# Kernel optimization log

Measured on AMD Instinct MI355X. Metric: run time of the kernel, lower is better.

Reference implementation:

```python
import jax, jax.numpy as jnp
import numpy as np

BATCH = 131072
NUM_OSC = 4
NUM_SPEC = 300
FREQ_LO, FREQ_HI = 0.5, 5.0


def setup_inputs() -> dict:
    key = jax.random.key(0)
    ks = jax.random.split(key, 8)
    return {
        "G": jax.random.normal(ks[0], (BATCH, 8), dtype=jnp.float32),
        "W1": jax.random.normal(ks[1], (100, 8), dtype=jnp.float32) * 0.3,
        "b1": jax.random.normal(ks[2], (100,), dtype=jnp.float32) * 0.1,
        "W2": jax.random.normal(ks[3], (100, 100), dtype=jnp.float32) * 0.1,
        "b2": jax.random.normal(ks[4], (100,), dtype=jnp.float32) * 0.1,
        "W_w0": jax.random.normal(ks[5], (NUM_OSC, 100), dtype=jnp.float32) * 0.1,
        "W_wp": jax.random.normal(ks[6], (NUM_OSC, 100), dtype=jnp.float32) * 0.1,
        # torch.nn.init.uniform_(lin_g.weight, a=0.0, b=0.1)
        "W_g": jax.random.uniform(ks[7], (NUM_OSC, 100), dtype=jnp.float32) * 0.1,
    }


def reference(G, W1, b1, W2, b2, W_w0, W_wp, W_g):
    # MLP trunk: 8 -> 100 -> 100, ReLU on both layers
    out = jax.nn.relu(G @ W1.T + b1)
    out = jax.nn.relu(out @ W2.T + b2)          # (B, 100)

    # Oscillator parameter heads (bias-free), ReLU-clamped, shape (B, 4, 1)
    w0 = jax.nn.relu(out @ W_w0.T)[:, :, None]
    wp = jax.nn.relu(out @ W_wp.T)[:, :, None]
    g = jax.nn.relu(out @ W_g.T)[:, :, None]

    # Frequency grid (300,) broadcast against (B, 4, 1)
    w = jnp.arange(FREQ_LO, FREQ_HI, (FREQ_HI - FREQ_LO) / NUM_SPEC, dtype=jnp.float32)

    # Lorentz oscillator imaginary permittivity
    num = (wp ** 2) * (w * g)                   # (B, 4, 300)
    den = (w0 ** 2 - w ** 2) ** 2 + (w ** 2) * (g ** 2)
    e2 = num / den
    return jnp.sum(e2, axis=1)                  # (B, 300)
```

## Files before the change

### kernel.cpp

```cpp
#include <hip/hip_runtime.h>

#define BATCH 131072
#define NS    300
#define H     100
#define BLK   256
#define EPB   64
#define NBLK  (BATCH / EPB)
#define NQ4   (EPB * NS / 4)
#define H2STR 112
#define LOOFF 14336

typedef __attribute__((ext_vector_type(8))) short bf16x8;
typedef __attribute__((ext_vector_type(4))) float f32x4;

__device__ __forceinline__ unsigned short f2bf(float f) {
    unsigned int u = __float_as_uint(f);
    return (unsigned short)((u + 0x7fffu + ((u >> 16) & 1u)) >> 16);
}
__device__ __forceinline__ float bf2f(unsigned short h) {
    return __uint_as_float(((unsigned int)h) << 16);
}

__global__ void prep_w2(const float* __restrict__ W2, unsigned short* __restrict__ wsb) {
    const int fi   = blockIdx.x * 4 + (threadIdx.x >> 6);
    const int lane = threadIdx.x & 63;
    const int s = fi / 7, t = fi % 7;
    const int n  = t * 16 + (lane & 15);
    const int k0 = s * 32 + ((lane >> 4) << 3);
    unsigned short* hi = wsb + ((size_t)fi * 64 + lane) * 8;
#pragma unroll
    for (int i = 0; i < 8; ++i) {
        const int k = k0 + i;
        const float v = (k < H && n < H) ? W2[n * H + k] : 0.f;
        const unsigned short h = f2bf(v);
        hi[i]         = h;
        hi[LOOFF + i] = f2bf(v - bf2f(h));
    }
}

__global__ void prep_small(const float* __restrict__ Ww0, const float* __restrict__ Wwp,
                           const float* __restrict__ Wg,  const float* __restrict__ b2,
                           float* __restrict__ hdt, float* __restrict__ b2p) {
    const int i = blockIdx.x * 256 + threadIdx.x;
    if (i < 12 * 112) {
        const int c = i / 112, j = i % 112;
        const float* src = (c < 4) ? Ww0 : (c < 8) ? Wwp : Wg;
        hdt[i] = (j < H) ? src[(c & 3) * H + j] : 0.f;
    }
    if (i < 112) b2p[i] = (i < H) ? b2[i] : 0.f;
}

__global__ __launch_bounds__(BLK)
void lorentz_fused(const float* __restrict__ G,   const float* __restrict__ W1,
                   const float* __restrict__ b1,  const unsigned short* __restrict__ wsb,
                   const float* __restrict__ hdt, const float* __restrict__ b2p,
                   float* __restrict__ out)
{
    __shared__ __align__(16) float h2buf[4][16][H2STR];
    __shared__ __align__(16) float sPP[EPB * 12];

    const int tid  = threadIdx.x;
    const int w    = tid >> 6, lane = tid & 63, ln = lane & 15, gr = lane >> 4;
    const int e0   = blockIdx.x * EPB + w * 16;

    const float4* gp = (const float4*)(G + (size_t)(e0 + ln) * 8);
    const float4 gA = gp[0], gB = gp[1];

    f32x4 acc[7];
#pragma unroll
    for (int t = 0; t < 7; ++t) acc[t] = (f32x4){0.f, 0.f, 0.f, 0.f};

    const bf16x8* Bf = (const bf16x8*)wsb;

#pragma unroll
    for (int s = 0; s < 4; ++s) {
        bf16x8 ahi, alo;
#pragma unroll
        for (int i = 0; i < 8; ++i) {
            const int k  = s * 32 + gr * 8 + i;
            const int kc = (k < H) ? k : (H - 1);
            const float4 ra = ((const float4*)(W1 + kc * 8))[0];
            const float4 rb = ((const float4*)(W1 + kc * 8))[1];
            float s0 = fmaf(gA.x, ra.x, b1[kc]);
            float s1 = gA.y * ra.y;
            s0 = fmaf(gA.z, ra.z, s0);  s1 = fmaf(gA.w, ra.w, s1);
            s0 = fmaf(gB.x, rb.x, s0);  s1 = fmaf(gB.y, rb.y, s1);
            s0 = fmaf(gB.z, rb.z, s0);  s1 = fmaf(gB.w, rb.w, s1);
            const float h = fmaxf(s0 + s1, 0.f);
            const unsigned short hh = f2bf(h);
            ahi[i] = (short)hh;
            alo[i] = (short)f2bf(h - bf2f(hh));
        }
#pragma unroll
        for (int t = 0; t < 7; ++t) {
            const bf16x8 bh = Bf[(s * 7 + t) * 64 + lane];
            const bf16x8 bl = Bf[1792 + (s * 7 + t) * 64 + lane];
            acc[t] = __builtin_amdgcn_mfma_f32_16x16x32_bf16(ahi, bh, acc[t], 0, 0, 0);
            acc[t] = __builtin_amdgcn_mfma_f32_16x16x32_bf16(ahi, bl, acc[t], 0, 0, 0);
            acc[t] = __builtin_amdgcn_mfma_f32_16x16x32_bf16(alo, bh, acc[t], 0, 0, 0);
        }
    }

#pragma unroll
    for (int t = 0; t < 7; ++t) {
        const float b2v = b2p[t * 16 + ln];
#pragma unroll
        for (int r = 0; r < 4; ++r)
            h2buf[w][gr * 4 + r][t * 16 + ln] = fmaxf(acc[t][r] + b2v, 0.f);
    }
    __syncthreads();

    {
        const int row = lane >> 2, q = lane & 3;
        const float4* h4 = (const float4*)&h2buf[w][row][0];
        const float4* d0 = (const float4*)(hdt + q * 112);
        const float4* d1 = (const float4*)(hdt + (4 + q) * 112);
        const float4* d2 = (const float4*)(hdt + (8 + q) * 112);
        float s0 = 0.f, s1 = 0.f, s2 = 0.f;
#pragma unroll
        for (int k4 = 0; k4 < 28; ++k4) {
            const float4 hv = h4[k4];
            const float4 a = d0[k4], b = d1[k4], c = d2[k4];
            s0 = fmaf(hv.x, a.x, s0); s1 = fmaf(hv.x, b.x, s1); s2 = fmaf(hv.x, c.x, s2);
            s0 = fmaf(hv.y, a.y, s0); s1 = fmaf(hv.y, b.y, s1); s2 = fmaf(hv.y, c.y, s2);
            s0 = fmaf(hv.z, a.z, s0); s1 = fmaf(hv.z, b.z, s1); s2 = fmaf(hv.z, c.z, s2);
            s0 = fmaf(hv.w, a.w, s0); s1 = fmaf(hv.w, b.w, s1); s2 = fmaf(hv.w, c.w, s2);
        }
        const float w0 = fmaxf(s0, 0.f), wp = fmaxf(s1, 0.f), gg = fmaxf(s2, 0.f);
        const int el = w * 16 + row;
        sPP[el * 12 + q]     = w0 * w0;
        sPP[el * 12 + 4 + q] = gg * gg;
        sPP[el * 12 + 8 + q] = wp * wp * gg;
    }
    __syncthreads();

    float4* out4 = (float4*)out;
    const size_t base4 = (size_t)blockIdx.x * NQ4;

#define SPEC(idx4)                                                              \
    {   const int e  = (idx4) / 75;                                             \
        const int k4 = (idx4) - e * 75;                                         \
        const float4 P0 = ((const float4*)(sPP + e * 12))[0];                   \
        const float4 P1 = ((const float4*)(sPP + e * 12))[1];                   \
        const float4 P2 = ((const float4*)(sPP + e * 12))[2];                   \
        const float kb = (float)(k4 << 2);                                      \
        float4 r; float* rp = (float*)&r;                                       \
        _Pragma("unroll")                                                       \
        for (int i = 0; i < 4; ++i) {                                           \
            const float w_  = 0.5f + (kb + (float)i) * 0.015f;                  \
            const float wsq = w_ * w_;                                          \
            const float t0 = P0.x - wsq, t1 = P0.y - wsq,                       \
                        t2 = P0.z - wsq, t3 = P0.w - wsq;                       \
            const float d0 = fmaf(t0, t0, wsq * P1.x);                          \
            const float d1 = fmaf(t1, t1, wsq * P1.y);                          \
            const float d2 = fmaf(t2, t2, wsq * P1.z);                          \
            const float d3 = fmaf(t3, t3, wsq * P1.w);                          \
            const float d01 = d0 * d1, d23 = d2 * d3;                           \
            const float D   = d01 * d23;                                        \
            const float n01 = fmaf(P2.y, d0, P2.x * d1);                        \
            const float n23 = fmaf(P2.w, d2, P2.z * d3);                        \
            const float N   = fmaf(n01, d23, n23 * d01);                        \
            rp[i] = w_ * (N * __builtin_amdgcn_rcpf(D));                        \
        }                                                                       \
        out4[base4 + (idx4)] = r; }

    for (int it = 0; it < NQ4 / BLK; ++it) {
        const int idx4 = it * BLK + tid;
        SPEC(idx4)
    }
    if (tid < NQ4 - (NQ4 / BLK) * BLK) {
        const int idx4 = (NQ4 / BLK) * BLK + tid;
        SPEC(idx4)
    }
#undef SPEC
}

extern "C" void kernel_launch(void* const* d_in, const int* in_sizes, int n_in,
                              void* d_out, int out_size, void* d_ws, size_t ws_size,
                              hipStream_t stream) {
    const float* G   = (const float*)d_in[0];
    const float* W1  = (const float*)d_in[1];
    const float* b1  = (const float*)d_in[2];
    const float* W2  = (const float*)d_in[3];
    const float* b2  = (const float*)d_in[4];
    const float* Ww0 = (const float*)d_in[5];
    const float* Wwp = (const float*)d_in[6];
    const float* Wg  = (const float*)d_in[7];
    float* out = (float*)d_out;

    unsigned short* wsb = (unsigned short*)d_ws;
    float* hdt = (float*)((char*)d_ws + 57344);
    float* b2p = (float*)((char*)d_ws + 57344 + 5376);

    prep_w2<<<7, 256, 0, stream>>>(W2, wsb);
    prep_small<<<6, 256, 0, stream>>>(Ww0, Wwp, Wg, b2, hdt, b2p);
    lorentz_fused<<<NBLK, BLK, 0, stream>>>(G, W1, b1, wsb, hdt, b2p, out);
}
```

Baseline: 100.6 us.

## Split fused kernel into MLP kernel and grid-stride spectrum kernel via workspace

The single fused kernel is split in two. The MLP/head kernel now writes per-element oscillator parameters (w0², g², wp²·g) to three global workspace arrays, and a separate grid-stride kernel computes the Lorentz spectrum and streams the output. This removes the block-level syncs and lets the store-heavy spectrum phase run at its own occupancy instead of being tied to the MLP kernel's register and LDS footprint. The cost is an extra launch and a small global round-trip for the parameters (about 6 MB).

```diff
diff --git a/kernel.cpp b/kernel.cpp
--- a/kernel.cpp
+++ b/kernel.cpp
@@ -6,9 +6,15 @@
 #define BLK   256
 #define EPB   64
 #define NBLK  (BATCH / EPB)
-#define NQ4   (EPB * NS / 4)
 #define H2STR 112
 #define LOOFF 14336
+
+#define WS_P0   0
+#define WS_P1   2097152
+#define WS_P2   4194304
+#define WS_WSB  6291456
+#define WS_HDT  6348800
+#define WS_B2P  6354176
 
 typedef __attribute__((ext_vector_type(8))) short bf16x8;
 typedef __attribute__((ext_vector_type(4))) float f32x4;
@@ -51,19 +57,18 @@
 }
 
 __global__ __launch_bounds__(BLK)
-void lorentz_fused(const float* __restrict__ G,   const float* __restrict__ W1,
-                   const float* __restrict__ b1,  const unsigned short* __restrict__ wsb,
-                   const float* __restrict__ hdt, const float* __restrict__ b2p,
-                   float* __restrict__ out)
+void lorentz_mlp(const float* __restrict__ G,   const float* __restrict__ W1,
+                 const float* __restrict__ b1,  const unsigned short* __restrict__ wsb,
+                 const float* __restrict__ hdt, const float* __restrict__ b2p,
+                 float* __restrict__ p0f, float* __restrict__ p1f, float* __restrict__ p2f)
 {
     __shared__ __align__(16) float h2buf[4][16][H2STR];
-    __shared__ __align__(16) float sPP[EPB * 12];
 
     const int tid  = threadIdx.x;
     const int w    = tid >> 6, lane = tid & 63, ln = lane & 15, gr = lane >> 4;
-    const int e0   = blockIdx.x * EPB + w * 16;
-
-    const float4* gp = (const float4*)(G + (size_t)(e0 + ln) * 8);
+    const int e0w  = blockIdx.x * EPB + w * 16;
+
+    const float4* gp = (const float4*)(G + (size_t)(e0w + ln) * 8);
     const float4 gA = gp[0], gB = gp[1];
 
     f32x4 acc[7];
@@ -108,7 +113,6 @@
         for (int r = 0; r < 4; ++r)
             h2buf[w][gr * 4 + r][t * 16 + ln] = fmaxf(acc[t][r] + b2v, 0.f);
     }
-    __syncthreads();
 
     {
         const int row = lane >> 2, q = lane & 3;
@@ -127,52 +131,48 @@
             s0 = fmaf(hv.w, a.w, s0); s1 = fmaf(hv.w, b.w, s1); s2 = fmaf(hv.w, c.w, s2);
         }
         const float w0 = fmaxf(s0, 0.f), wp = fmaxf(s1, 0.f), gg = fmaxf(s2, 0.f);
-        const int el = w * 16 + row;
-        sPP[el * 12 + q]     = w0 * w0;
-        sPP[el * 12 + 4 + q] = gg * gg;
-        sPP[el * 12 + 8 + q] = wp * wp * gg;
-    }
-    __syncthreads();
-
-    float4* out4 = (float4*)out;
-    const size_t base4 = (size_t)blockIdx.x * NQ4;
-
-#define SPEC(idx4)                                                              \
-    {   const int e  = (idx4) / 75;                                             \
-        const int k4 = (idx4) - e * 75;                                         \
-        const float4 P0 = ((const float4*)(sPP + e * 12))[0];                   \
-        const float4 P1 = ((const float4*)(sPP + e * 12))[1];                   \
-        const float4 P2 = ((const float4*)(sPP + e * 12))[2];                   \
-        const float kb = (float)(k4 << 2);                                      \
-        float4 r; float* rp = (float*)&r;                                       \
-        _Pragma("unroll")                                                       \
-        for (int i = 0; i < 4; ++i) {                                           \
-            const float w_  = 0.5f + (kb + (float)i) * 0.015f;                  \
-            const float wsq = w_ * w_;                                          \
-            const float t0 = P0.x - wsq, t1 = P0.y - wsq,                       \
-                        t2 = P0.z - wsq, t3 = P0.w - wsq;                       \
-            const float d0 = fmaf(t0, t0, wsq * P1.x);                          \
-            const float d1 = fmaf(t1, t1, wsq * P1.y);                          \
-            const float d2 = fmaf(t2, t2, wsq * P1.z);                          \
-            const float d3 = fmaf(t3, t3, wsq * P1.w);                          \
-            const float d01 = d0 * d1, d23 = d2 * d3;                           \
-            const float D   = d01 * d23;                                        \
-            const float n01 = fmaf(P2.y, d0, P2.x * d1);                        \
-            const float n23 = fmaf(P2.w, d2, P2.z * d3);                        \
-            const float N   = fmaf(n01, d23, n23 * d01);                        \
-            rp[i] = w_ * (N * __builtin_amdgcn_rcpf(D));                        \
-        }                                                                       \
-        out4[base4 + (idx4)] = r; }
-
-    for (int it = 0; it < NQ4 / BLK; ++it) {
-        const int idx4 = it * BLK + tid;
-        SPEC(idx4)
-    }
-    if (tid < NQ4 - (NQ4 / BLK) * BLK) {
-        const int idx4 = (NQ4 / BLK) * BLK + tid;
-        SPEC(idx4)
-    }
-#undef SPEC
+        const int gi = e0w * 4 + lane;
+        p0f[gi] = w0 * w0;
+        p1f[gi] = gg * gg;
+        p2f[gi] = wp * wp * gg;
+    }
+}
+
+#define SGRID 2048
+#define NQTOT (BATCH * NS / 4)
+
+__global__ __launch_bounds__(BLK)
+void lorentz_spec(const float4* __restrict__ p0g, const float4* __restrict__ p1g,
+                  const float4* __restrict__ p2g, float4* __restrict__ out4)
+{
+    int idx = blockIdx.x * BLK + threadIdx.x;
+    const int stride = SGRID * BLK;
+#pragma unroll 1
+    for (; idx < NQTOT; idx += stride) {
+        const int e  = idx / 75;
+        const int k4 = idx - e * 75;
+        const float4 P0 = p0g[e], P1 = p1g[e], P2 = p2g[e];
+        const float kb = (float)(k4 << 2);
+        float4 r; float* rp = (float*)&r;
+#pragma unroll
+        for (int i = 0; i < 4; ++i) {
+            const float w_  = 0.5f + (kb + (float)i) * 0.015f;
+            const float wsq = w_ * w_;
+            const float t0 = P0.x - wsq, t1 = P0.y - wsq,
+                        t2 = P0.z - wsq, t3 = P0.w - wsq;
+            const float d0 = fmaf(t0, t0, wsq * P1.x);
+            const float d1 = fmaf(t1, t1, wsq * P1.y);
+            const float d2 = fmaf(t2, t2, wsq * P1.z);
+            const float d3 = fmaf(t3, t3, wsq * P1.w);
+            const float d01 = d0 * d1, d23 = d2 * d3;
+            const float D   = d01 * d23;
+            const float n01 = fmaf(P2.y, d0, P2.x * d1);
+            const float n23 = fmaf(P2.w, d2, P2.z * d3);
+            const float N   = fmaf(n01, d23, n23 * d01);
+            rp[i] = w_ * (N * __builtin_amdgcn_rcpf(D));
+        }
+        out4[idx] = r;
+    }
 }
 
 extern "C" void kernel_launch(void* const* d_in, const int* in_sizes, int n_in,
@@ -188,11 +188,17 @@
     const float* Wg  = (const float*)d_in[7];
     float* out = (float*)d_out;
 
-    unsigned short* wsb = (unsigned short*)d_ws;
-    float* hdt = (float*)((char*)d_ws + 57344);
-    float* b2p = (float*)((char*)d_ws + 57344 + 5376);
+    char* ws = (char*)d_ws;
+    float*          p0f = (float*)(ws + WS_P0);
+    float*          p1f = (float*)(ws + WS_P1);
+    float*          p2f = (float*)(ws + WS_P2);
+    unsigned short* wsb = (unsigned short*)(ws + WS_WSB);
+    float*          hdt = (float*)(ws + WS_HDT);
+    float*          b2p = (float*)(ws + WS_B2P);
 
     prep_w2<<<7, 256, 0, stream>>>(W2, wsb);
     prep_small<<<6, 256, 0, stream>>>(Ww0, Wwp, Wg, b2, hdt, b2p);
-    lorentz_fused<<<NBLK, BLK, 0, stream>>>(G, W1, b1, wsb, hdt, b2p, out);
-}
+    lorentz_mlp<<<NBLK, BLK, 0, stream>>>(G, W1, b1, wsb, hdt, b2p, p0f, p1f, p2f);
+    lorentz_spec<<<SGRID, BLK, 0, stream>>>((const float4*)p0f, (const float4*)p1f,
+                                            (const float4*)p2f, (float4*)out);
+}
```

New measurement: 115.9 us. 15.2% more time.
